# Kernel tuning notes

Measured on AMD Instinct MI355X. Metric: run time of the kernel, lower is better.

The kernel has to match this reference:

```python
import jax, jax.numpy as jnp
import numpy as np

# Gemma-2B-like config
B, S = 2, 2048
HIDDEN = 2048
N_HEADS = 8
N_KV_HEADS = 1
HEAD_DIM = 256
INTER = 16384
EPS = 1e-6
SCALING = HEAD_DIM ** -0.5
NEG_INF = -1e9


def rms_norm(x, w, eps=EPS):
    xf = x.astype(jnp.float32)
    n = xf * jax.lax.rsqrt(jnp.mean(xf * xf, axis=-1, keepdims=True) + eps)
    return n.astype(x.dtype) * (1.0 + w)


def apply_rope(x, cos, sin):
    # x: [B, S, H, D]; cos/sin: [S, D/2] -> broadcast [1, S, 1, D/2]
    d2 = x.shape[-1] // 2
    x1, x2 = x[..., :d2], x[..., d2:]
    c = cos[None, :, None, :]
    s = sin[None, :, None, :]
    return jnp.concatenate([x1 * c - x2 * s, x1 * s + x2 * c], axis=-1)


def setup_inputs() -> dict:
    key = jax.random.key(0)
    ks = jax.random.split(key, 12)
    std = 0.02
    hidden_states = jax.random.normal(ks[0], (B, S, HIDDEN), jnp.float32)
    # rotary embeddings
    inv_freq = 1.0 / (10000.0 ** (np.arange(0, HEAD_DIM, 2, dtype=np.float32) / HEAD_DIM))
    t = np.arange(S, dtype=np.float32)
    freqs = np.outer(t, inv_freq)  # [S, D/2]
    freqs_cos = jnp.asarray(np.cos(freqs))
    freqs_sin = jnp.asarray(np.sin(freqs))
    kv_write_indices = jnp.arange(S, dtype=jnp.int32)
    k_cache = jnp.zeros((B, S, N_KV_HEADS, HEAD_DIM), jnp.float32)
    v_cache = jnp.zeros((B, S, N_KV_HEADS, HEAD_DIM), jnp.float32)
    causal = np.triu(np.full((S, S), NEG_INF, dtype=np.float32), k=1)
    mask = jnp.asarray(causal)[None, None, :, :]  # [1,1,S,S]
    q_w = jax.random.normal(ks[1], (N_HEADS * HEAD_DIM, HIDDEN), jnp.float32) * std
    k_w = jax.random.normal(ks[2], (N_KV_HEADS * HEAD_DIM, HIDDEN), jnp.float32) * std
    v_w = jax.random.normal(ks[3], (N_KV_HEADS * HEAD_DIM, HIDDEN), jnp.float32) * std
    o_w = jax.random.normal(ks[4], (HIDDEN, N_HEADS * HEAD_DIM), jnp.float32) * std
    gate_w = jax.random.normal(ks[5], (INTER, HIDDEN), jnp.float32) * std
    up_w = jax.random.normal(ks[6], (INTER, HIDDEN), jnp.float32) * std
    down_w = jax.random.normal(ks[7], (HIDDEN, INTER), jnp.float32) * std
    ln1_w = jax.random.normal(ks[8], (HIDDEN,), jnp.float32) * 0.1
    ln2_w = jax.random.normal(ks[9], (HIDDEN,), jnp.float32) * 0.1
    return dict(hidden_states=hidden_states, freqs_cos=freqs_cos, freqs_sin=freqs_sin,
                kv_write_indices=kv_write_indices, k_cache=k_cache, v_cache=v_cache, mask=mask,
                q_w=q_w, k_w=k_w, v_w=v_w, o_w=o_w, gate_w=gate_w, up_w=up_w, down_w=down_w,
                ln1_w=ln1_w, ln2_w=ln2_w)


def decoder_layer(hidden_states, freqs_cos, freqs_sin, kv_write_indices, k_cache, v_cache, mask,
                  q_w, k_w, v_w, o_w, gate_w, up_w, down_w, ln1_w, ln2_w):
    b, s, _ = hidden_states.shape
    g = N_HEADS // N_KV_HEADS  # queries per kv head
    # --- attention block ---
    residual = hidden_states
    h = rms_norm(hidden_states, ln1_w)
    xq = (h @ q_w.T).reshape(b, s, N_HEADS, HEAD_DIM)
    xk = (h @ k_w.T).reshape(b, s, N_KV_HEADS, HEAD_DIM)
    xv = (h @ v_w.T).reshape(b, s, N_KV_HEADS, HEAD_DIM)
    xq = apply_rope(xq, freqs_cos, freqs_sin)
    xk = apply_rope(xk, freqs_cos, freqs_sin)
    # KV-cache write (index_copy along time dim)
    k_cache = k_cache.at[:, kv_write_indices].set(xk)
    v_cache = v_cache.at[:, kv_write_indices].set(xv)
    c = k_cache.shape[1]
    # GQA: avoid materializing repeated heads; group queries per kv head
    qg = xq.reshape(b, s, N_KV_HEADS, g, HEAD_DIM)
    scores = jnp.einsum('bshgd,bchd->bhgsc', qg, k_cache) * SCALING  # [B,Hk,G,S,C]
    scores = scores.reshape(b, N_HEADS, s, c) + mask
    probs = jax.nn.softmax(scores.astype(jnp.float32), axis=-1).astype(xq.dtype)
    probs = probs.reshape(b, N_KV_HEADS, g, s, c)
    out = jnp.einsum('bhgsc,bchd->bshgd', probs, v_cache).reshape(b, s, N_HEADS * HEAD_DIM)
    attn_out = out @ o_w.T
    hidden_states = residual + attn_out
    # --- MLP block (GeGLU) ---
    residual = hidden_states
    h = rms_norm(hidden_states, ln2_w)
    gate = jax.nn.gelu(h @ gate_w.T, approximate=True)
    up = h @ up_w.T
    hidden_states = residual + (gate * up) @ down_w.T
    return hidden_states


def reference(hidden_states, freqs_cos, freqs_sin, kv_write_indices, k_cache, v_cache, mask,
              q_w, k_w, v_w, o_w, gate_w, up_w, down_w, ln1_w, ln2_w):
    return decoder_layer(hidden_states, freqs_cos, freqs_sin, kv_write_indices, k_cache, v_cache,
                         mask, q_w, k_w, v_w, o_w, gate_w, up_w, down_w, ln1_w, ln2_w)
```

## Files before the change

### kernel.cpp

```cpp
#include <hip/hip_runtime.h>

typedef __bf16 bf16;
typedef __bf16 bf16x8 __attribute__((ext_vector_type(8)));
typedef float  f32x4  __attribute__((ext_vector_type(4)));

#define BATCH  2
#define SEQ    2048
#define HIDDEN 2048
#define NHEADS 8
#define HD     256
#define INTER  16384
#define EPS    1e-6f
#define SCALING 0.0625f

#define DT_BF16 0
#define DT_F32  1
#define DT_PROBE 2

__device__ __forceinline__ bool dt_is_f32(int code, const unsigned* probe) {
    if (code == DT_PROBE) return probe[0] == 0x3F800000u;
    return code == DT_F32;
}

__device__ __forceinline__ void load8f(const void* p, long idx, bool f32, float* o) {
    if (f32) {
        const float* q = (const float*)p + idx;
        float4 a = *(const float4*)q;
        float4 b = *(const float4*)(q + 4);
        o[0]=a.x; o[1]=a.y; o[2]=a.z; o[3]=a.w;
        o[4]=b.x; o[5]=b.y; o[6]=b.z; o[7]=b.w;
    } else {
        bf16x8 v = *(const bf16x8*)((const bf16*)p + idx);
#pragma unroll
        for (int i = 0; i < 8; ++i) o[i] = (float)v[i];
    }
}

__device__ __forceinline__ void store8(void* p, long idx, bool f32, const float* v) {
    if (f32) {
        float* q = (float*)p + idx;
        *(float4*)q       = make_float4(v[0], v[1], v[2], v[3]);
        *(float4*)(q + 4) = make_float4(v[4], v[5], v[6], v[7]);
    } else {
        bf16x8 o;
#pragma unroll
        for (int i = 0; i < 8; ++i) o[i] = (bf16)v[i];
        *(bf16x8*)((bf16*)p + idx) = o;
    }
}

__device__ __forceinline__ void gl2lds16(const void* g, void* l) {
    __builtin_amdgcn_global_load_lds(
        (const __attribute__((address_space(1))) void*)(unsigned long long)g,
        (__attribute__((address_space(3))) void*)(unsigned)(unsigned long long)l,
        16, 0, 0);
}

template <bool BF32, bool FUSE_GELU>
__device__ __forceinline__ void gemm_body(
    const bf16* __restrict__ A, const void* __restrict__ B, void* __restrict__ C,
    int M, int N, int K, int lda, int ldb, int ldc,
    long aoff, long boff, long coff, bool cf32, char* smem)
{
    bf16* As = (bf16*)smem;
    char* Bs = smem + 16384;

    const int tid  = threadIdx.x;
    const int wid  = tid >> 6;
    const int lane = tid & 63;
    const int quad = lane >> 4;
    const int l16  = lane & 15;

    const int gx = gridDim.x, gy = gridDim.y;
    const int nwg  = gx * gy;
    const int orig = blockIdx.y * gx + blockIdx.x;
    const int q8 = nwg >> 3, r8 = nwg & 7;
    const int xc = orig & 7, oo = orig >> 3;
    const int wg = (xc < r8 ? xc * (q8 + 1) : r8 * (q8 + 1) + (xc - r8) * q8) + oo;
    const int m0 = (wg / gx) * 128;
    const int n0 = (wg % gx) * 128;

    f32x4 acc[4][4];
#pragma unroll
    for (int i = 0; i < 4; ++i)
#pragma unroll
        for (int j = 0; j < 4; ++j) acc[i][j] = (f32x4){0.f, 0.f, 0.f, 0.f};

    const int wm = (wid >> 1) << 6;
    const int wn = (wid & 1) << 6;

    for (int k0 = 0; k0 < K; k0 += 64) {
#pragma unroll
        for (int i = 0; i < 4; ++i) {
            const int b   = i * 4096 + wid * 1024 + lane * 16;
            const int row = b >> 7;
            const int sb  = b ^ ((row & 7) << 4);
            const int col = (sb & 127) >> 1;
            gl2lds16(A + aoff + (long)(m0 + row) * lda + (k0 + col),
                     smem + i * 4096 + wid * 1024);
        }
        if (BF32) {
            const float* Bp = (const float*)B;
#pragma unroll
            for (int i = 0; i < 8; ++i) {
                const int b   = i * 4096 + wid * 1024 + lane * 16;
                const int row = b >> 8;
                const int sb  = b ^ ((row & 15) << 4);
                const int col = (sb & 255) >> 2;
                gl2lds16(Bp + boff + (long)(n0 + row) * ldb + (k0 + col),
                         Bs + i * 4096 + wid * 1024);
            }
        } else {
            const bf16* Bp = (const bf16*)B;
#pragma unroll
            for (int i = 0; i < 4; ++i) {
                const int b   = i * 4096 + wid * 1024 + lane * 16;
                const int row = b >> 7;
                const int sb  = b ^ ((row & 7) << 4);
                const int col = (sb & 127) >> 1;
                gl2lds16(Bp + boff + (long)(n0 + row) * ldb + (k0 + col),
                         Bs + i * 4096 + wid * 1024);
            }
        }
        __syncthreads();

#pragma unroll
        for (int kk = 0; kk < 64; kk += 32) {
            bf16x8 af[4], bfr[4];
#pragma unroll
            for (int i = 0; i < 4; ++i) {
                const int row = wm + i * 16 + l16;
                const int byt = ((row << 7) + (kk << 1) + (quad << 4))
                                ^ ((row & 7) << 4);
                af[i] = *(const bf16x8*)(smem + byt);
            }
            if (BF32) {
#pragma unroll
                for (int j = 0; j < 4; ++j) {
                    const int row  = wn + j * 16 + l16;
                    const int base = (row << 8) + (kk << 2) + (quad << 5);
                    const int swz  = (row & 15) << 4;
                    const f32x4 lo = *(const f32x4*)(Bs + (base ^ swz));
                    const f32x4 hi = *(const f32x4*)(Bs + ((base + 16) ^ swz));
                    bf16x8 t;
                    t[0]=(bf16)lo[0]; t[1]=(bf16)lo[1]; t[2]=(bf16)lo[2]; t[3]=(bf16)lo[3];
                    t[4]=(bf16)hi[0]; t[5]=(bf16)hi[1]; t[6]=(bf16)hi[2]; t[7]=(bf16)hi[3];
                    bfr[j] = t;
                }
            } else {
#pragma unroll
                for (int j = 0; j < 4; ++j) {
                    const int row = wn + j * 16 + l16;
                    const int byt = ((row << 7) + (kk << 1) + (quad << 4))
                                    ^ ((row & 7) << 4);
                    bfr[j] = *(const bf16x8*)(Bs + byt);
                }
            }
#pragma unroll
            for (int i = 0; i < 4; ++i)
#pragma unroll
                for (int j = 0; j < 4; ++j)
                    acc[i][j] = __builtin_amdgcn_mfma_f32_16x16x32_bf16(
                        af[i], bfr[j], acc[i][j], 0, 0, 0);
        }
        __syncthreads();
    }

    bf16*  Cb = (bf16*)C  + coff;
    float* Cf = (float*)C + coff;
#pragma unroll
    for (int i = 0; i < 4; ++i)
#pragma unroll
        for (int j = 0; j < 4; ++j) {
            const int row = m0 + wm + i * 16 + quad * 4;
            const int col = n0 + wn + j * 16 + l16;
#pragma unroll
            for (int r = 0; r < 4; ++r) {
                const long idx = (long)(row + r) * ldc + col;
                if (FUSE_GELU) {
                    const float g = (float)Cb[idx];
                    const float t = tanhf(0.7978845608028654f *
                                          (g + 0.044715f * g * g * g));
                    Cb[idx] = (bf16)(0.5f * g * (1.0f + t) * acc[i][j][r]);
                } else if (cf32) {
                    Cf[idx] = acc[i][j][r];
                } else {
                    Cb[idx] = (bf16)acc[i][j][r];
                }
            }
        }
}

template <bool FUSE_GELU>
__global__ __launch_bounds__(256, 2)
void gemm_bt(const bf16* __restrict__ A, const void* __restrict__ B,
             void* __restrict__ C,
             int M, int N, int K, int lda, int ldb, int ldc,
             long sA1, long sA2, long sB1, long sB2, long sC1, long sC2,
             int nh, const unsigned* __restrict__ probe, int bcode, int ccode)
{
    __shared__ __attribute__((aligned(16))) char smem[49152];

    const int z  = blockIdx.z;
    const int zo = z / nh;
    const int zi = z - zo * nh;
    const long aoff = (long)zo * sA1 + (long)zi * sA2;
    const long boff = (long)zo * sB1 + (long)zi * sB2;
    const long coff = (long)zo * sC1 + (long)zi * sC2;
    const bool cf32 = (ccode == DT_F32);

    if (dt_is_f32(bcode, probe))
        gemm_body<true, FUSE_GELU>(A, B, C, M, N, K, lda, ldb, ldc,
                                   aoff, boff, coff, cf32, smem);
    else
        gemm_body<false, FUSE_GELU>(A, B, C, M, N, K, lda, ldb, ldc,
                                    aoff, boff, coff, cf32, smem);
}

__global__ __launch_bounds__(256)
void cvt_bf16(const void* __restrict__ in, bf16* __restrict__ out, long n,
              const unsigned* __restrict__ probe)
{
    const bool f = dt_is_f32(DT_PROBE, probe);
    const long i = ((long)blockIdx.x * 256 + threadIdx.x) * 8;
    if (i >= n) return;
    float v[8];
    load8f(in, i, f, v);
    bf16x8 o;
#pragma unroll
    for (int j = 0; j < 8; ++j) o[j] = (bf16)v[j];
    *(bf16x8*)(out + i) = o;
}

__global__ __launch_bounds__(256)
void rmsnorm_kernel(const void* __restrict__ x, const void* __restrict__ w,
                    bf16* __restrict__ out, const unsigned* __restrict__ probe,
                    int xcode)
{
    __shared__ float sred[8];
    const bool xf = dt_is_f32(xcode, probe);
    const bool wf = dt_is_f32(DT_PROBE, probe);
    const long t = blockIdx.x;
    const int c0 = threadIdx.x * 8;

    float xv[8];
    load8f(x, t * HIDDEN + c0, xf, xv);
    float ss = 0.f;
#pragma unroll
    for (int i = 0; i < 8; ++i) ss += xv[i] * xv[i];

    for (int off = 32; off; off >>= 1) ss += __shfl_down(ss, off, 64);
    const int wid = threadIdx.x >> 6, lane = threadIdx.x & 63;
    if (lane == 0) sred[wid] = ss;
    __syncthreads();
    if (threadIdx.x == 0)
        sred[4] = rsqrtf((sred[0] + sred[1] + sred[2] + sred[3]) / (float)HIDDEN + EPS);
    __syncthreads();
    const float inv = sred[4];

    float wv[8];
    load8f(w, c0, wf, wv);
    bf16x8 o8;
#pragma unroll
    for (int i = 0; i < 8; ++i) {
        const float n = (float)(bf16)(xv[i] * inv);
        o8[i] = (bf16)(n * (1.0f + wv[i]));
    }
    *(bf16x8*)(out + t * HIDDEN + c0) = o8;
}

__global__ __launch_bounds__(256)
void rope_kernel(bf16* __restrict__ x, const void* __restrict__ cosb,
                 const void* __restrict__ sinb,
                 const unsigned* __restrict__ probe, int nheads)
{
    const bool f = dt_is_f32(DT_PROBE, probe);
    const long idx = (long)blockIdx.x * 256 + threadIdx.x;
    const long total = (long)BATCH * SEQ * nheads * 128;
    if (idx >= total) return;
    const int d = (int)(idx & 127);
    const long r = idx >> 7;
    const long sh = r / nheads;
    const int s = (int)(sh & (SEQ - 1));
    bf16* p = x + r * 256;
    const float x1 = (float)p[d], x2 = (float)p[d + 128];
    const long fi = (long)s * 128 + d;
    const float c  = f ? ((const float*)cosb)[fi] : (float)((const bf16*)cosb)[fi];
    const float sn = f ? ((const float*)sinb)[fi] : (float)((const bf16*)sinb)[fi];
    p[d]       = (bf16)(x1 * c - x2 * sn);
    p[d + 128] = (bf16)(x1 * sn + x2 * c);
}

__global__ __launch_bounds__(256)
void transpose_kernel(const bf16* __restrict__ v, bf16* __restrict__ vt)
{
    __shared__ bf16 tile[32][33];
    const int b  = blockIdx.z;
    const int c0 = blockIdx.x * 32;
    const int d0 = blockIdx.y * 32;
    const int tx = threadIdx.x & 31, ty = threadIdx.x >> 5;
#pragma unroll
    for (int i = 0; i < 32; i += 8)
        tile[ty + i][tx] = v[((long)b * SEQ + c0 + ty + i) * HD + d0 + tx];
    __syncthreads();
#pragma unroll
    for (int i = 0; i < 32; i += 8)
        vt[((long)b * HD + d0 + ty + i) * SEQ + c0 + tx] = tile[tx][ty + i];
}

__global__ __launch_bounds__(256)
void softmax_kernel(bf16* __restrict__ sc)
{
    __shared__ float sred[8];
    const int s = blockIdx.x;
    bf16* row = sc + ((long)blockIdx.y * SEQ + s) * (long)SEQ;
    const int c0 = threadIdx.x * 8;

    bf16x8 v8 = *(const bf16x8*)(row + c0);
    float v[8];
    float m = -1e30f;
#pragma unroll
    for (int i = 0; i < 8; ++i) {
        const float fv = (float)v8[i] * SCALING;
        v[i] = (c0 + i <= s) ? fv : -1e30f;
        m = fmaxf(m, v[i]);
    }
    for (int off = 32; off; off >>= 1) m = fmaxf(m, __shfl_down(m, off, 64));
    const int wid = threadIdx.x >> 6, lane = threadIdx.x & 63;
    if (lane == 0) sred[wid] = m;
    __syncthreads();
    if (threadIdx.x == 0)
        sred[4] = fmaxf(fmaxf(sred[0], sred[1]), fmaxf(sred[2], sred[3]));
    __syncthreads();
    m = sred[4];

    float p[8], sum = 0.f;
#pragma unroll
    for (int i = 0; i < 8; ++i) {
        p[i] = (c0 + i <= s) ? expf(v[i] - m) : 0.f;
        sum += p[i];
    }
    for (int off = 32; off; off >>= 1) sum += __shfl_down(sum, off, 64);
    __syncthreads();
    if (lane == 0) sred[wid] = sum;
    __syncthreads();
    if (threadIdx.x == 0) sred[5] = sred[0] + sred[1] + sred[2] + sred[3];
    __syncthreads();
    const float inv = 1.0f / sred[5];

    bf16x8 o8;
#pragma unroll
    for (int i = 0; i < 8; ++i) o8[i] = (bf16)(p[i] * inv);
    *(bf16x8*)(row + c0) = o8;
}

__global__ __launch_bounds__(256)
void add_kernel(const void* __restrict__ a, const void* __restrict__ b,
                void* __restrict__ o, long n, const unsigned* __restrict__ probe,
                int acode, int bcode, int ocode)
{
    const bool af = dt_is_f32(acode, probe);
    const bool bf = dt_is_f32(bcode, probe);
    const bool of = dt_is_f32(ocode, probe);
    const long i = ((long)blockIdx.x * 256 + threadIdx.x) * 8;
    if (i >= n) return;
    float av[8], bv[8], ov[8];
    load8f(a, i, af, av);
    load8f(b, i, bf, bv);
#pragma unroll
    for (int j = 0; j < 8; ++j) ov[j] = av[j] + bv[j];
    store8(o, i, of, ov);
}

extern "C" void kernel_launch(void* const* d_in, const int* in_sizes, int n_in,
                              void* d_out, int out_size, void* d_ws, size_t ws_size,
                              hipStream_t stream)
{
    const void* hs   = d_in[0];
    const void* fcos = d_in[1];
    const void* fsin = d_in[2];
    const void* qw   = d_in[7];
    const void* kw   = d_in[8];
    const void* vw   = d_in[9];
    const void* ow   = d_in[10];
    const void* gw   = d_in[11];
    const void* uw   = d_in[12];
    const void* dw   = d_in[13];
    const void* ln1  = d_in[14];
    const void* ln2  = d_in[15];
    const unsigned* probe = (const unsigned*)fcos;

    char* ws = (char*)d_ws;
    const size_t MB = 1ull << 20;
    bf16*  sc   = (bf16*)(ws);
    bf16*  h1   = (bf16*)(ws + 128 * MB);
    bf16*  n2   = (bf16*)(ws + 128 * MB);
    bf16*  xq   = (bf16*)(ws + 144 * MB);
    bf16*  hid2 = (bf16*)(ws + 144 * MB);
    bf16*  xk   = (bf16*)(ws + 160 * MB);
    bf16*  xv   = (bf16*)(ws + 162 * MB);
    bf16*  vt   = (bf16*)(ws + 164 * MB);
    bf16*  ao   = (bf16*)(ws + 166 * MB);
    float* dp   = (float*)(ws + 160 * MB);
    bf16*  op   = (bf16*)(ws + 182 * MB);

    bf16* qwb = (bf16*)(ws + 198 * MB);
    bf16* kwb = qwb + (long)HIDDEN * HIDDEN;
    bf16* vwb = kwb + (long)HD * HIDDEN;
    bf16* owb = vwb + (long)HD * HIDDEN;
    bf16* gwb = owb + (long)HIDDEN * HIDDEN;
    bf16* uwb = gwb + (long)INTER * HIDDEN;
    bf16* dwb = uwb + (long)INTER * HIDDEN;
    const bool cvt = ws_size >= 198 * MB + 220200960ull;

    const long NTOK = (long)BATCH * SEQ;
    const long NELT = NTOK * HIDDEN;

    if (cvt) {
        cvt_bf16<<<dim3(2048),  256, 0, stream>>>(qw, qwb, (long)HIDDEN * HIDDEN, probe);
        cvt_bf16<<<dim3(256),   256, 0, stream>>>(kw, kwb, (long)HD * HIDDEN, probe);
        cvt_bf16<<<dim3(256),   256, 0, stream>>>(vw, vwb, (long)HD * HIDDEN, probe);
        cvt_bf16<<<dim3(2048),  256, 0, stream>>>(ow, owb, (long)HIDDEN * HIDDEN, probe);
        cvt_bf16<<<dim3(16384), 256, 0, stream>>>(gw, gwb, (long)INTER * HIDDEN, probe);
        cvt_bf16<<<dim3(16384), 256, 0, stream>>>(uw, uwb, (long)INTER * HIDDEN, probe);
        cvt_bf16<<<dim3(16384), 256, 0, stream>>>(dw, dwb, (long)INTER * HIDDEN, probe);
    }
    const void* QW = cvt ? (const void*)qwb : qw;
    const void* KW = cvt ? (const void*)kwb : kw;
    const void* VW = cvt ? (const void*)vwb : vw;
    const void* OW = cvt ? (const void*)owb : ow;
    const void* GW = cvt ? (const void*)gwb : gw;
    const void* UW = cvt ? (const void*)uwb : uw;
    const void* DW = cvt ? (const void*)dwb : dw;
    const int wcode = cvt ? DT_BF16 : DT_PROBE;

    rmsnorm_kernel<<<dim3(NTOK), 256, 0, stream>>>(hs, ln1, h1, probe, DT_PROBE);

    gemm_bt<false><<<dim3(HIDDEN / 128, NTOK / 128, 1), 256, 0, stream>>>(
        h1, QW, xq, (int)NTOK, HIDDEN, HIDDEN, HIDDEN, HIDDEN, HIDDEN,
        0, 0, 0, 0, 0, 0, 1, probe, wcode, DT_BF16);
    gemm_bt<false><<<dim3(HD / 128, NTOK / 128, 1), 256, 0, stream>>>(
        h1, KW, xk, (int)NTOK, HD, HIDDEN, HIDDEN, HIDDEN, HD,
        0, 0, 0, 0, 0, 0, 1, probe, wcode, DT_BF16);
    gemm_bt<false><<<dim3(HD / 128, NTOK / 128, 1), 256, 0, stream>>>(
        h1, VW, xv, (int)NTOK, HD, HIDDEN, HIDDEN, HIDDEN, HD,
        0, 0, 0, 0, 0, 0, 1, probe, wcode, DT_BF16);

    rope_kernel<<<dim3(16384), 256, 0, stream>>>(xq, fcos, fsin, probe, NHEADS);
    rope_kernel<<<dim3(2048), 256, 0, stream>>>(xk, fcos, fsin, probe, 1);

    transpose_kernel<<<dim3(SEQ / 32, HD / 32, BATCH), 256, 0, stream>>>(xv, vt);

    gemm_bt<false><<<dim3(SEQ / 128, SEQ / 128, BATCH * NHEADS), 256, 0, stream>>>(
        xq, xk, sc, SEQ, SEQ, HD, NHEADS * HD, HD, SEQ,
        (long)SEQ * NHEADS * HD, (long)HD,
        (long)SEQ * HD, 0L,
        (long)NHEADS * SEQ * SEQ, (long)SEQ * SEQ, NHEADS,
        probe, DT_BF16, DT_BF16);

    softmax_kernel<<<dim3(SEQ, BATCH * NHEADS), 256, 0, stream>>>(sc);

    gemm_bt<false><<<dim3(HD / 128, SEQ / 128, BATCH * NHEADS), 256, 0, stream>>>(
        sc, vt, ao, SEQ, HD, SEQ, SEQ, SEQ, NHEADS * HD,
        (long)NHEADS * SEQ * SEQ, (long)SEQ * SEQ,
        (long)HD * SEQ, 0L,
        (long)SEQ * NHEADS * HD, (long)HD, NHEADS,
        probe, DT_BF16, DT_BF16);

    gemm_bt<false><<<dim3(HIDDEN / 128, NTOK / 128, 1), 256, 0, stream>>>(
        ao, OW, op, (int)NTOK, HIDDEN, HIDDEN, HIDDEN, HIDDEN, HIDDEN,
        0, 0, 0, 0, 0, 0, 1, probe, wcode, DT_BF16);
    add_kernel<<<dim3((unsigned)(NELT / 2048)), 256, 0, stream>>>(
        hs, op, hid2, NELT, probe, DT_PROBE, DT_BF16, DT_BF16);

    rmsnorm_kernel<<<dim3(NTOK), 256, 0, stream>>>(hid2, ln2, n2, probe, DT_BF16);

    gemm_bt<false><<<dim3(INTER / 128, NTOK / 128, 1), 256, 0, stream>>>(
        n2, GW, sc, (int)NTOK, INTER, HIDDEN, HIDDEN, HIDDEN, INTER,
        0, 0, 0, 0, 0, 0, 1, probe, wcode, DT_BF16);
    gemm_bt<true><<<dim3(INTER / 128, NTOK / 128, 1), 256, 0, stream>>>(
        n2, UW, sc, (int)NTOK, INTER, HIDDEN, HIDDEN, HIDDEN, INTER,
        0, 0, 0, 0, 0, 0, 1, probe, wcode, DT_BF16);

    gemm_bt<false><<<dim3(HIDDEN / 128, NTOK / 128, 1), 256, 0, stream>>>(
        sc, DW, dp, (int)NTOK, HIDDEN, INTER, INTER, INTER, HIDDEN,
        0, 0, 0, 0, 0, 0, 1, probe, wcode, DT_F32);
    add_kernel<<<dim3((unsigned)(NELT / 2048)), 256, 0, stream>>>(
        dp, hid2, d_out, NELT, probe, DT_F32, DT_BF16, DT_PROBE);
}
```

Before: 1.856 ms.

## Add 256x256 tiled GEMM kernel for MLP and QK^T, split-K down projection

Introduces a 512-thread GEMM with 256x256 output tiles, a double-buffered 128KB LDS layout with XOR swizzle, and interleaved staging, barriers and setprio scheduling. It is used for the QK^T scores and for the gate, up and down MLP projections when the bf16 weight copies exist. The down projection splits K in two, writing two fp32 partials that a new three-input add kernel sums with the residual. gemm_bt now uses dynamic shared memory so the bf16-weight path requests only 32KB, which may allow higher occupancy. The larger tiles cut global traffic per FLOP, at the cost of one block per CU and an extra fp32 partial buffer pass.

```diff
diff --git a/kernel.cpp b/kernel.cpp
--- a/kernel.cpp
+++ b/kernel.cpp
@@ -62,7 +62,6 @@
     int M, int N, int K, int lda, int ldb, int ldc,
     long aoff, long boff, long coff, bool cf32, char* smem)
 {
-    bf16* As = (bf16*)smem;
     char* Bs = smem + 16384;
 
     const int tid  = threadIdx.x;
@@ -71,8 +70,8 @@
     const int quad = lane >> 4;
     const int l16  = lane & 15;
 
-    const int gx = gridDim.x, gy = gridDim.y;
-    const int nwg  = gx * gy;
+    const int gx = gridDim.x;
+    const int nwg  = gx * gridDim.y;
     const int orig = blockIdx.y * gx + blockIdx.x;
     const int q8 = nwg >> 3, r8 = nwg & 7;
     const int xc = orig & 7, oo = orig >> 3;
@@ -199,7 +198,7 @@
              long sA1, long sA2, long sB1, long sB2, long sC1, long sC2,
              int nh, const unsigned* __restrict__ probe, int bcode, int ccode)
 {
-    __shared__ __attribute__((aligned(16))) char smem[49152];
+    extern __shared__ char smem[];
 
     const int z  = blockIdx.z;
     const int zo = z / nh;
@@ -215,6 +214,176 @@
     else
         gemm_body<false, FUSE_GELU>(A, B, C, M, N, K, lda, ldb, ldc,
                                     aoff, boff, coff, cf32, smem);
+}
+
+template <bool FUSE_GELU>
+__global__ __launch_bounds__(512, 1)
+void gemm256(const bf16* __restrict__ A, const bf16* __restrict__ B,
+             void* __restrict__ C,
+             int M, int N, int K, int lda, int ldb, int ldc,
+             long sA1, long sA2, long sB1, long sB2, long sC1, long sC2,
+             int nh, int ccode)
+{
+    __shared__ __attribute__((aligned(16))) char smem[131072];
+
+    const int tid    = threadIdx.x;
+    const int wid    = tid >> 6;
+    const int lane   = tid & 63;
+    const int quad   = lane >> 4;
+    const int l16    = lane & 15;
+    const int warp_m = wid >> 2;
+    const int warp_n = wid & 3;
+    const int wm     = warp_m << 7;
+    const int wn     = warp_n << 6;
+    const int Xa     = (l16 & 7) << 4;
+
+    const int z  = blockIdx.z;
+    const int zo = z / nh;
+    const int zi = z - zo * nh;
+    const long aoff = (long)zo * sA1 + (long)zi * sA2;
+    const long boff = (long)zo * sB1 + (long)zi * sB2;
+    const long coff = (long)zo * sC1 + (long)zi * sC2;
+    const bool cf32 = (ccode == DT_F32);
+
+    const int gx   = gridDim.x;
+    const int nwg  = gx * gridDim.y;
+    const int orig = blockIdx.y * gx + blockIdx.x;
+    const int q8 = nwg >> 3, r8 = nwg & 7;
+    const int xc = orig & 7, oo = orig >> 3;
+    const int wg = (xc < r8 ? xc * (q8 + 1) : r8 * (q8 + 1) + (xc - r8) * q8) + oo;
+    const int m0 = (wg / gx) * 256;
+    const int n0 = (wg % gx) * 256;
+
+    const int prow = tid >> 3;
+    const int pcol = (((tid & 7) << 4) ^ ((prow & 7) << 4)) >> 1;
+
+    f32x4 acc[8][4];
+#pragma unroll
+    for (int i = 0; i < 8; ++i)
+#pragma unroll
+        for (int j = 0; j < 4; ++j) acc[i][j] = (f32x4){0.f, 0.f, 0.f, 0.f};
+
+#define STAGE_A(POS, TS, BUF) do {                                             \
+    const long g_ = aoff + (long)(m0 + (POS)*128 + prow) * lda                 \
+                    + ((TS)*64 + pcol);                                        \
+    char* d_ = smem + ((BUF) << 16) + (POS)*16384 + wid*1024;                  \
+    gl2lds16(A + g_, d_);                                                      \
+    gl2lds16(A + g_ + (long)64 * lda, d_ + 8192); } while (0)
+
+#define STAGE_B(POS, TS, BUF) do {                                             \
+    const long g_ = boff + (long)(n0 + ((POS)-2)*128 + prow) * ldb             \
+                    + ((TS)*64 + pcol);                                        \
+    char* d_ = smem + ((BUF) << 16) + (POS)*16384 + wid*1024;                  \
+    gl2lds16(B + g_, d_);                                                      \
+    gl2lds16(B + g_ + (long)64 * ldb, d_ + 8192); } while (0)
+
+#define LDA_(dst, RH, BUFO)                                                    \
+    _Pragma("unroll") for (int ii = 0; ii < 4; ++ii)                           \
+    _Pragma("unroll") for (int kk = 0; kk < 2; ++kk) {                         \
+        const int adr_ = (((RH)*64 + ii*16 + l16) << 7)                        \
+                         | (((kk << 6) | (quad << 4)) ^ Xa);                   \
+        dst[ii][kk] = *(const bf16x8*)(smem + (BUFO) + warp_m*16384 + adr_); }
+
+#define LDB_(dst, NH, BUFO)                                                    \
+    _Pragma("unroll") for (int jj = 0; jj < 2; ++jj)                           \
+    _Pragma("unroll") for (int kk = 0; kk < 2; ++kk) {                         \
+        const int adr_ = ((((warp_n & 1)*64) + (NH)*32 + jj*16 + l16) << 7)    \
+                         | (((kk << 6) | (quad << 4)) ^ Xa);                   \
+        dst[jj][kk] = *(const bf16x8*)(smem + (BUFO)                           \
+                         + (2 + (warp_n >> 1))*16384 + adr_); }
+
+#define MM_(RH, NH, AR, BR)                                                    \
+    _Pragma("unroll") for (int ii = 0; ii < 4; ++ii)                           \
+    _Pragma("unroll") for (int jj = 0; jj < 2; ++jj)                           \
+    _Pragma("unroll") for (int kk = 0; kk < 2; ++kk)                           \
+        acc[(RH)*4 + ii][(NH)*2 + jj] =                                        \
+            __builtin_amdgcn_mfma_f32_16x16x32_bf16(                           \
+                AR[ii][kk], BR[jj][kk], acc[(RH)*4 + ii][(NH)*2 + jj], 0,0,0);
+
+    const int NT = K >> 6;
+
+    STAGE_A(0, 0, 0); STAGE_A(1, 0, 0); STAGE_B(2, 0, 0); STAGE_B(3, 0, 0);
+    STAGE_A(0, 1, 1); STAGE_A(1, 1, 1);
+    asm volatile("s_waitcnt vmcnt(4)" ::: "memory");
+    __builtin_amdgcn_s_barrier();
+
+    bf16x8 a0[4][2], a1[4][2], b0f[2][2], b1f[2][2];
+
+    for (int t = 0; t < NT; ++t) {
+        const int buf  = t & 1;
+        const int bufo = buf << 16;
+        const int nbuf = buf ^ 1;
+        const int ts1  = (t + 1 < NT) ? t + 1 : t + 1 - NT;
+        const int ts2  = (t + 2 < NT) ? t + 2 : t + 2 - NT;
+
+        LDA_(a0, 0, bufo); LDB_(b0f, 0, bufo);
+        STAGE_B(2, ts1, nbuf);
+        __builtin_amdgcn_s_barrier();
+        asm volatile("s_waitcnt lgkmcnt(0)" ::: "memory");
+        __builtin_amdgcn_sched_barrier(0);
+        __builtin_amdgcn_s_setprio(1);
+        MM_(0, 0, a0, b0f);
+        __builtin_amdgcn_s_setprio(0);
+        __builtin_amdgcn_s_barrier();
+
+        LDA_(a1, 1, bufo);
+        STAGE_B(3, ts1, nbuf);
+        __builtin_amdgcn_s_barrier();
+        asm volatile("s_waitcnt lgkmcnt(0)" ::: "memory");
+        __builtin_amdgcn_sched_barrier(0);
+        __builtin_amdgcn_s_setprio(1);
+        MM_(1, 0, a1, b0f);
+        __builtin_amdgcn_s_setprio(0);
+        __builtin_amdgcn_s_barrier();
+
+        LDB_(b1f, 1, bufo);
+        STAGE_A(0, ts2, buf);
+        __builtin_amdgcn_s_barrier();
+        asm volatile("s_waitcnt lgkmcnt(0)" ::: "memory");
+        __builtin_amdgcn_sched_barrier(0);
+        __builtin_amdgcn_s_setprio(1);
+        MM_(1, 1, a1, b1f);
+        __builtin_amdgcn_s_setprio(0);
+        __builtin_amdgcn_s_barrier();
+
+        STAGE_A(1, ts2, buf);
+        __builtin_amdgcn_s_setprio(1);
+        MM_(0, 1, a0, b1f);
+        __builtin_amdgcn_s_setprio(0);
+        asm volatile("s_waitcnt vmcnt(4)" ::: "memory");
+        __builtin_amdgcn_s_barrier();
+    }
+    asm volatile("s_waitcnt vmcnt(0) lgkmcnt(0)" ::: "memory");
+
+#undef STAGE_A
+#undef STAGE_B
+#undef LDA_
+#undef LDB_
+#undef MM_
+
+    bf16*  Cb = (bf16*)C  + coff;
+    float* Cf = (float*)C + coff;
+#pragma unroll
+    for (int ii = 0; ii < 8; ++ii)
+#pragma unroll
+        for (int jj = 0; jj < 4; ++jj) {
+            const int row = m0 + wm + ii * 16 + quad * 4;
+            const int col = n0 + wn + jj * 16 + l16;
+#pragma unroll
+            for (int r = 0; r < 4; ++r) {
+                const long idx = (long)(row + r) * ldc + col;
+                if (FUSE_GELU) {
+                    const float g = (float)Cb[idx];
+                    const float th = tanhf(0.7978845608028654f *
+                                           (g + 0.044715f * g * g * g));
+                    Cb[idx] = (bf16)(0.5f * g * (1.0f + th) * acc[ii][jj][r]);
+                } else if (cf32) {
+                    Cf[idx] = acc[ii][jj][r];
+                } else {
+                    Cb[idx] = (bf16)acc[ii][jj][r];
+                }
+            }
+        }
 }
 
 __global__ __launch_bounds__(256)
@@ -372,6 +541,23 @@
     store8(o, i, of, ov);
 }
 
+__global__ __launch_bounds__(256)
+void add3_kernel(const float* __restrict__ a, const float* __restrict__ b,
+                 const bf16* __restrict__ c, void* __restrict__ o, long n,
+                 const unsigned* __restrict__ probe)
+{
+    const bool of = dt_is_f32(DT_PROBE, probe);
+    const long i = ((long)blockIdx.x * 256 + threadIdx.x) * 8;
+    if (i >= n) return;
+    float av[8], bv[8], ov[8];
+    load8f(a, i, true, av);
+    load8f(b, i, true, bv);
+    bf16x8 cv = *(const bf16x8*)(c + i);
+#pragma unroll
+    for (int j = 0; j < 8; ++j) ov[j] = av[j] + bv[j] + (float)cv[j];
+    store8(o, i, of, ov);
+}
+
 extern "C" void kernel_launch(void* const* d_in, const int* in_sizes, int n_in,
                               void* d_out, int out_size, void* d_ws, size_t ws_size,
                               hipStream_t stream)
@@ -401,7 +587,6 @@
     bf16*  xv   = (bf16*)(ws + 162 * MB);
     bf16*  vt   = (bf16*)(ws + 164 * MB);
     bf16*  ao   = (bf16*)(ws + 166 * MB);
-    float* dp   = (float*)(ws + 160 * MB);
     bf16*  op   = (bf16*)(ws + 182 * MB);
 
     bf16* qwb = (bf16*)(ws + 198 * MB);
@@ -413,6 +598,9 @@
     bf16* dwb = uwb + (long)INTER * HIDDEN;
     const bool cvt = ws_size >= 198 * MB + 220200960ull;
 
+    float* dp0 = (float*)(ws + (cvt ? 192 : 160) * MB);
+    float* dp1 = (float*)(ws + 224 * MB);
+
     const long NTOK = (long)BATCH * SEQ;
     const long NELT = NTOK * HIDDEN;
 
@@ -429,20 +617,18 @@
     const void* KW = cvt ? (const void*)kwb : kw;
     const void* VW = cvt ? (const void*)vwb : vw;
     const void* OW = cvt ? (const void*)owb : ow;
-    const void* GW = cvt ? (const void*)gwb : gw;
-    const void* UW = cvt ? (const void*)uwb : uw;
-    const void* DW = cvt ? (const void*)dwb : dw;
     const int wcode = cvt ? DT_BF16 : DT_PROBE;
+    const unsigned shW = cvt ? 32768u : 49152u;
 
     rmsnorm_kernel<<<dim3(NTOK), 256, 0, stream>>>(hs, ln1, h1, probe, DT_PROBE);
 
-    gemm_bt<false><<<dim3(HIDDEN / 128, NTOK / 128, 1), 256, 0, stream>>>(
+    gemm_bt<false><<<dim3(HIDDEN / 128, NTOK / 128, 1), 256, shW, stream>>>(
         h1, QW, xq, (int)NTOK, HIDDEN, HIDDEN, HIDDEN, HIDDEN, HIDDEN,
         0, 0, 0, 0, 0, 0, 1, probe, wcode, DT_BF16);
-    gemm_bt<false><<<dim3(HD / 128, NTOK / 128, 1), 256, 0, stream>>>(
+    gemm_bt<false><<<dim3(HD / 128, NTOK / 128, 1), 256, shW, stream>>>(
         h1, KW, xk, (int)NTOK, HD, HIDDEN, HIDDEN, HIDDEN, HD,
         0, 0, 0, 0, 0, 0, 1, probe, wcode, DT_BF16);
-    gemm_bt<false><<<dim3(HD / 128, NTOK / 128, 1), 256, 0, stream>>>(
+    gemm_bt<false><<<dim3(HD / 128, NTOK / 128, 1), 256, shW, stream>>>(
         h1, VW, xv, (int)NTOK, HD, HIDDEN, HIDDEN, HIDDEN, HD,
         0, 0, 0, 0, 0, 0, 1, probe, wcode, DT_BF16);
 
@@ -451,23 +637,22 @@
 
     transpose_kernel<<<dim3(SEQ / 32, HD / 32, BATCH), 256, 0, stream>>>(xv, vt);
 
-    gemm_bt<false><<<dim3(SEQ / 128, SEQ / 128, BATCH * NHEADS), 256, 0, stream>>>(
+    gemm256<false><<<dim3(SEQ / 256, SEQ / 256, BATCH * NHEADS), 512, 0, stream>>>(
         xq, xk, sc, SEQ, SEQ, HD, NHEADS * HD, HD, SEQ,
         (long)SEQ * NHEADS * HD, (long)HD,
         (long)SEQ * HD, 0L,
-        (long)NHEADS * SEQ * SEQ, (long)SEQ * SEQ, NHEADS,
-        probe, DT_BF16, DT_BF16);
+        (long)NHEADS * SEQ * SEQ, (long)SEQ * SEQ, NHEADS, DT_BF16);
 
     softmax_kernel<<<dim3(SEQ, BATCH * NHEADS), 256, 0, stream>>>(sc);
 
-    gemm_bt<false><<<dim3(HD / 128, SEQ / 128, BATCH * NHEADS), 256, 0, stream>>>(
+    gemm_bt<false><<<dim3(HD / 128, SEQ / 128, BATCH * NHEADS), 256, 32768, stream>>>(
         sc, vt, ao, SEQ, HD, SEQ, SEQ, SEQ, NHEADS * HD,
         (long)NHEADS * SEQ * SEQ, (long)SEQ * SEQ,
         (long)HD * SEQ, 0L,
         (long)SEQ * NHEADS * HD, (long)HD, NHEADS,
         probe, DT_BF16, DT_BF16);
 
-    gemm_bt<false><<<dim3(HIDDEN / 128, NTOK / 128, 1), 256, 0, stream>>>(
+    gemm_bt<false><<<dim3(HIDDEN / 128, NTOK / 128, 1), 256, shW, stream>>>(
         ao, OW, op, (int)NTOK, HIDDEN, HIDDEN, HIDDEN, HIDDEN, HIDDEN,
         0, 0, 0, 0, 0, 0, 1, probe, wcode, DT_BF16);
     add_kernel<<<dim3((unsigned)(NELT / 2048)), 256, 0, stream>>>(
@@ -475,16 +660,30 @@
 
     rmsnorm_kernel<<<dim3(NTOK), 256, 0, stream>>>(hid2, ln2, n2, probe, DT_BF16);
 
-    gemm_bt<false><<<dim3(INTER / 128, NTOK / 128, 1), 256, 0, stream>>>(
-        n2, GW, sc, (int)NTOK, INTER, HIDDEN, HIDDEN, HIDDEN, INTER,
-        0, 0, 0, 0, 0, 0, 1, probe, wcode, DT_BF16);
-    gemm_bt<true><<<dim3(INTER / 128, NTOK / 128, 1), 256, 0, stream>>>(
-        n2, UW, sc, (int)NTOK, INTER, HIDDEN, HIDDEN, HIDDEN, INTER,
-        0, 0, 0, 0, 0, 0, 1, probe, wcode, DT_BF16);
-
-    gemm_bt<false><<<dim3(HIDDEN / 128, NTOK / 128, 1), 256, 0, stream>>>(
-        sc, DW, dp, (int)NTOK, HIDDEN, INTER, INTER, INTER, HIDDEN,
-        0, 0, 0, 0, 0, 0, 1, probe, wcode, DT_F32);
-    add_kernel<<<dim3((unsigned)(NELT / 2048)), 256, 0, stream>>>(
-        dp, hid2, d_out, NELT, probe, DT_F32, DT_BF16, DT_PROBE);
-}
+    if (cvt) {
+        gemm256<false><<<dim3(INTER / 256, NTOK / 256, 1), 512, 0, stream>>>(
+            n2, gwb, sc, (int)NTOK, INTER, HIDDEN, HIDDEN, HIDDEN, INTER,
+            0, 0, 0, 0, 0, 0, 1, DT_BF16);
+        gemm256<true><<<dim3(INTER / 256, NTOK / 256, 1), 512, 0, stream>>>(
+            n2, uwb, sc, (int)NTOK, INTER, HIDDEN, HIDDEN, HIDDEN, INTER,
+            0, 0, 0, 0, 0, 0, 1, DT_BF16);
+        gemm256<false><<<dim3(HIDDEN / 256, NTOK / 256, 2), 512, 0, stream>>>(
+            sc, dwb, dp0, (int)NTOK, HIDDEN, INTER / 2, INTER, INTER, HIDDEN,
+            (long)(INTER / 2), 0L, (long)(INTER / 2), 0L,
+            (long)NTOK * HIDDEN, 0L, 1, DT_F32);
+        add3_kernel<<<dim3((unsigned)(NELT / 2048)), 256, 0, stream>>>(
+            dp0, dp1, hid2, d_out, NELT, probe);
+    } else {
+        gemm_bt<false><<<dim3(INTER / 128, NTOK / 128, 1), 256, 49152, stream>>>(
+            n2, gw, sc, (int)NTOK, INTER, HIDDEN, HIDDEN, HIDDEN, INTER,
+            0, 0, 0, 0, 0, 0, 1, probe, DT_PROBE, DT_BF16);
+        gemm_bt<true><<<dim3(INTER / 128, NTOK / 128, 1), 256, 49152, stream>>>(
+            n2, uw, sc, (int)NTOK, INTER, HIDDEN, HIDDEN, HIDDEN, INTER,
+            0, 0, 0, 0, 0, 0, 1, probe, DT_PROBE, DT_BF16);
+        gemm_bt<false><<<dim3(HIDDEN / 128, NTOK / 128, 1), 256, 49152, stream>>>(
+            sc, dw, dp0, (int)NTOK, HIDDEN, INTER, INTER, INTER, HIDDEN,
+            0, 0, 0, 0, 0, 0, 1, probe, DT_PROBE, DT_F32);
+        add_kernel<<<dim3((unsigned)(NELT / 2048)), 256, 0, stream>>>(
+            dp0, hid2, d_out, NELT, probe, DT_F32, DT_BF16, DT_PROBE);
+    }
+}
```

After: 1.711 ms. -7.8%, faster.
